# Kernel optimization log

Hardware: AMD Instinct MI355X
Metric: run time of the kernel (lower is better)

The kernel has to match this reference:

```python
import jax, jax.numpy as jnp
import numpy as np

NEG_SLOPE = 0.2  # PyG GATConv default LeakyReLU slope
BN_EPS = 1e-5


def gat_layer(x, src, dst, W, a_src, a_dst, num_nodes):
    """PyG-style GATConv (no dropout, eval mode). Returns [N, H, C]."""
    H, C = a_src.shape
    h = (x @ W).reshape(-1, H, C)                       # [N,H,C]
    s_src = jnp.einsum('nhc,hc->nh', h, a_src)          # [N,H]
    s_dst = jnp.einsum('nhc,hc->nh', h, a_dst)          # [N,H]
    e = jax.nn.leaky_relu(s_src[src] + s_dst[dst], NEG_SLOPE)  # [E,H]
    # segment softmax over incoming edges of each dst node
    e_max = jax.ops.segment_max(e, dst, num_segments=num_nodes)  # [N,H]
    e_exp = jnp.exp(e - e_max[dst])
    denom = jax.ops.segment_sum(e_exp, dst, num_segments=num_nodes)
    alpha = e_exp / (denom[dst] + 1e-16)                # [E,H]
    msg = h[src] * alpha[:, :, None]                    # [E,H,C] (dominant intermediate)
    return jax.ops.segment_sum(msg, dst, num_segments=num_nodes)  # [N,H,C]


def setup_inputs() -> dict:
    key = jax.random.key(0)
    ks = jax.random.split(key, 12)
    N, Din, Hdim, Heads, Dout = 50000, 128, 128, 8, 128
    E = 150000
    inp = {}
    inp['x'] = jax.random.normal(ks[0], (N, Din), dtype=jnp.float32)
    inp['edge_index'] = jax.random.randint(ks[1], (2, E), 0, N, dtype=jnp.int64)
    sc1 = 1.0 / np.sqrt(Din)
    inp['W1'] = jax.random.uniform(ks[2], (Din, Heads * Hdim), minval=-sc1, maxval=sc1, dtype=jnp.float32)
    inp['a_src1'] = jax.random.normal(ks[3], (Heads, Hdim), dtype=jnp.float32) * 0.1
    inp['a_dst1'] = jax.random.normal(ks[4], (Heads, Hdim), dtype=jnp.float32) * 0.1
    inp['b1'] = jnp.zeros((Heads * Hdim,), dtype=jnp.float32)
    inp['gamma'] = jnp.ones((Heads * Hdim,), dtype=jnp.float32)
    inp['beta'] = jnp.zeros((Heads * Hdim,), dtype=jnp.float32)
    sc2 = 1.0 / np.sqrt(Heads * Hdim)
    inp['W2'] = jax.random.uniform(ks[5], (Heads * Hdim, Dout), minval=-sc2, maxval=sc2, dtype=jnp.float32)
    inp['a_src2'] = jax.random.normal(ks[6], (1, Dout), dtype=jnp.float32) * 0.1
    inp['a_dst2'] = jax.random.normal(ks[7], (1, Dout), dtype=jnp.float32) * 0.1
    inp['b2'] = jnp.zeros((Dout,), dtype=jnp.float32)
    return inp


def reference(x, W1, a_src1, a_dst1, b1, gamma, beta, W2, a_src2, a_dst2, b2, edge_index):
    N = x.shape[0]
    src, dst = edge_index[0], edge_index[1]
    # GAT layer 1: heads=8, concat=True
    h1 = gat_layer(x, src, dst, W1, a_src1, a_dst1, N)   # [N,8,128]
    h1 = h1.reshape(N, -1) + b1                          # [N,1024]
    # BatchNorm1d (training-mode batch stats, biased variance as in torch)
    mu = jnp.mean(h1, axis=0)
    var = jnp.var(h1, axis=0)
    h1 = gamma * (h1 - mu) * jax.lax.rsqrt(var + BN_EPS) + beta
    h1 = jax.nn.elu(h1)
    # GAT layer 2: heads=1, concat=False (mean == squeeze for 1 head)
    h2 = gat_layer(h1, src, dst, W2, a_src2, a_dst2, N)  # [N,1,128]
    return h2[:, 0, :] + b2
```

## Files before the change

kernel.cpp:

```cpp
#include <hip/hip_runtime.h>
#include <hip/hip_bf16.h>
#include <math.h>

#define NEG_SLOPE 0.2f
#define BN_EPS 1e-5f

typedef short bf16x8 __attribute__((ext_vector_type(8)));
typedef float f32x4 __attribute__((ext_vector_type(4)));

__device__ __forceinline__ float bf2f(unsigned short u) {
  union { unsigned int i; float f; } v;
  v.i = ((unsigned int)u) << 16;
  return v.f;
}
__device__ __forceinline__ unsigned short f2bf(float f) {
  union { unsigned int i; float f; } v;
  v.f = f;
  unsigned int i = v.i;
  unsigned int r = (i + 0x7fffu + ((i >> 16) & 1u)) >> 16;
  return (unsigned short)r;
}

__global__ __launch_bounds__(256) void detect_kernel(
    const unsigned int* __restrict__ xw, const unsigned int* __restrict__ eiw,
    int E, int* __restrict__ flags) {
  __shared__ int cnt[2];
  if (threadIdx.x < 2) cnt[threadIdx.x] = 0;
  __syncthreads();
  int t = threadIdx.x;
  int inrange = 0;
  for (int i = t; i < 2048; i += 256) {
    unsigned int e = (xw[i] >> 7) & 0xFFu;
    inrange += (e >= 100u && e <= 135u) ? 1 : 0;
  }
  atomicAdd(&cnt[0], inrange);
  int M = min(1024, E / 2);
  int zeros = 0;
  for (int i = t; i < M; i += 256) zeros += (eiw[2 * i + 1] == 0u) ? 1 : 0;
  atomicAdd(&cnt[1], zeros);
  __syncthreads();
  if (t == 0) {
    flags[0] = (cnt[0] > 1536) ? 1 : 0;
    flags[1] = (cnt[1] > M / 2) ? 1 : 0;
  }
}

__global__ __launch_bounds__(256) void canon_x8(
    const void* __restrict__ src, unsigned short* __restrict__ dst, int n_real,
    int n_total, const int* __restrict__ flags) {
  int i = (blockIdx.x * 256 + threadIdx.x) * 8;
  if (i >= n_total) return;
  union { bf16x8 v; unsigned short u[8]; } o;
  if (i < n_real) {
    if (flags[0]) {
      o.v = *(const bf16x8*)((const unsigned short*)src + i);
    } else {
      const float4* f = (const float4*)((const float*)src + i);
      float4 f0 = f[0];
      float4 f1 = f[1];
      o.u[0] = f2bf(f0.x); o.u[1] = f2bf(f0.y);
      o.u[2] = f2bf(f0.z); o.u[3] = f2bf(f0.w);
      o.u[4] = f2bf(f1.x); o.u[5] = f2bf(f1.y);
      o.u[6] = f2bf(f1.z); o.u[7] = f2bf(f1.w);
    }
  } else {
#pragma unroll
    for (int j = 0; j < 8; ++j) o.u[j] = 0;
  }
  *(bf16x8*)(dst + i) = o.v;
}

__global__ __launch_bounds__(256) void canon_w_t(
    const void* __restrict__ src, unsigned short* __restrict__ dst, int Kdim,
    int Ndim, const int* __restrict__ flags) {
  int i = blockIdx.x * 256 + threadIdx.x;
  if (i >= Kdim * Ndim) return;
  int k = i / Ndim, n = i - k * Ndim;
  unsigned short v = flags[0] ? ((const unsigned short*)src)[i]
                              : f2bf(((const float*)src)[i]);
  dst[(size_t)n * Kdim + k] = v;
}

__global__ __launch_bounds__(1024) void canon_params(
    const void* s0, const void* s1, const void* s2, const void* s3,
    const void* s4, const void* s5, const void* s6, const void* s7,
    unsigned short* d0, unsigned short* d1, unsigned short* d2,
    unsigned short* d3, unsigned short* d4, unsigned short* d5,
    unsigned short* d6, unsigned short* d7, const int* __restrict__ flags) {
  int b = blockIdx.x, t = threadIdx.x;
  const void* s;
  unsigned short* d;
  int n;
  switch (b) {
    case 0: s = s0; d = d0; n = 1024; break;
    case 1: s = s1; d = d1; n = 1024; break;
    case 2: s = s2; d = d2; n = 1024; break;
    case 3: s = s3; d = d3; n = 1024; break;
    case 4: s = s4; d = d4; n = 1024; break;
    case 5: s = s5; d = d5; n = 128; break;
    case 6: s = s6; d = d6; n = 128; break;
    default: s = s7; d = d7; n = 128; break;
  }
  if (t < n)
    d[t] = flags[0] ? ((const unsigned short*)s)[t]
                    : f2bf(((const float*)s)[t]);
}

__global__ __launch_bounds__(256) void canon_idx(
    const int* __restrict__ ei, int* __restrict__ eis, int* __restrict__ eid,
    int E, const int* __restrict__ flags) {
  int e = blockIdx.x * 256 + threadIdx.x;
  if (e >= E) return;
  if (flags[1]) {
    eis[e] = ei[2 * (size_t)e];
    eid[e] = ei[2 * (size_t)E + 2 * (size_t)e];
  } else {
    eis[e] = ei[e];
    eid[e] = ei[E + e];
  }
}

template <int BM, bool TRANSFORM_A, bool OUT_BF16, bool SCORES>
__global__ __launch_bounds__(256) void gemm_mfma(
    const unsigned short* __restrict__ A, const unsigned short* __restrict__ Bt,
    void* __restrict__ Cv, int M, int N, int K,
    const float* __restrict__ scale, const float* __restrict__ shift,
    const unsigned short* __restrict__ aScr,
    const unsigned short* __restrict__ aDcr, float* __restrict__ ssrc,
    float* __restrict__ sdst, int hs) {
  constexpr int BK = 32;
  constexpr int LDA = BK + 8;
  constexpr int MI = BM / 32;
  __shared__ unsigned short As[BM * LDA];
  __shared__ unsigned short Bs[128 * LDA];
  __shared__ float sS[2][128];
  __shared__ float sD[2][128];

  const int m0 = blockIdx.y * BM;
  const int n0 = blockIdx.x * 128;
  const int tid = threadIdx.x;
  const int wid = tid >> 6;
  const int lane = tid & 63;
  const int q = lane >> 4;
  const int r = lane & 15;
  const int wm = (wid >> 1) * (BM / 2);
  const int wn = (wid & 1) * 64;

  f32x4 acc[MI][4] = {};

  const int row0 = (tid * 8) >> 5, col0 = (tid * 8) & 31;

  bf16x8 ra[2], rb[2];
  ra[0] = *(const bf16x8*)(A + (size_t)(m0 + row0) * K + col0);
  if (BM == 128)
    ra[1] = *(const bf16x8*)(A + (size_t)(m0 + row0 + 64) * K + col0);
  rb[0] = *(const bf16x8*)(Bt + (size_t)(n0 + row0) * K + col0);
  rb[1] = *(const bf16x8*)(Bt + (size_t)(n0 + row0 + 64) * K + col0);

  for (int k0 = 0; k0 < K; k0 += BK) {
#pragma unroll
    for (int rd = 0; rd < 2; ++rd) {
      int row = row0 + rd * 64;
      if (rd == 0 || BM == 128) {
        bf16x8 v = ra[rd];
        if (TRANSFORM_A) {
          float scv[8], shv[8];
          *(float4*)&scv[0] = *(const float4*)(scale + k0 + col0);
          *(float4*)&scv[4] = *(const float4*)(scale + k0 + col0 + 4);
          *(float4*)&shv[0] = *(const float4*)(shift + k0 + col0);
          *(float4*)&shv[4] = *(const float4*)(shift + k0 + col0 + 4);
          union { bf16x8 v; unsigned short u[8]; } p;
          p.v = v;
#pragma unroll
          for (int j = 0; j < 8; ++j) {
            float f = bf2f(p.u[j]) * scv[j] + shv[j];
            f = f > 0.f ? f : (__expf(f) - 1.0f);
            p.u[j] = f2bf(f);
          }
          v = p.v;
        }
        *(bf16x8*)(&As[row * LDA + col0]) = v;
      }
      *(bf16x8*)(&Bs[row * LDA + col0]) = rb[rd];
    }
    __syncthreads();

    int k1 = k0 + BK;
    if (k1 < K) {
      ra[0] = *(const bf16x8*)(A + (size_t)(m0 + row0) * K + k1 + col0);
      if (BM == 128)
        ra[1] = *(const bf16x8*)(A + (size_t)(m0 + row0 + 64) * K + k1 + col0);
      rb[0] = *(const bf16x8*)(Bt + (size_t)(n0 + row0) * K + k1 + col0);
      rb[1] = *(const bf16x8*)(Bt + (size_t)(n0 + row0 + 64) * K + k1 + col0);
    }

    bf16x8 af[MI], bfv[4];
#pragma unroll
    for (int mi = 0; mi < MI; ++mi)
      af[mi] = *(const bf16x8*)(&As[(wm + mi * 16 + r) * LDA + q * 8]);
#pragma unroll
    for (int ni = 0; ni < 4; ++ni)
      bfv[ni] = *(const bf16x8*)(&Bs[(wn + ni * 16 + r) * LDA + q * 8]);
#pragma unroll
    for (int mi = 0; mi < MI; ++mi)
#pragma unroll
      for (int ni = 0; ni < 4; ++ni)
        acc[mi][ni] = __builtin_amdgcn_mfma_f32_16x16x32_bf16(
            af[mi], bfv[ni], acc[mi][ni], 0, 0, 0);
    __syncthreads();
  }

#pragma unroll
  for (int mi = 0; mi < MI; ++mi) {
#pragma unroll
    for (int ni = 0; ni < 4; ++ni) {
#pragma unroll
      for (int i = 0; i < 4; ++i) {
        int row = m0 + wm + mi * 16 + q * 4 + i;
        int col = n0 + wn + ni * 16 + r;
        if (OUT_BF16)
          ((unsigned short*)Cv)[(size_t)row * N + col] = f2bf(acc[mi][ni][i]);
        else
          ((float*)Cv)[(size_t)row * N + col] = acc[mi][ni][i];
      }
    }
  }

  if (SCORES) {
    const int half = wid & 1;
    float aSv[4], aDv[4];
#pragma unroll
    for (int ni = 0; ni < 4; ++ni) {
      aSv[ni] = bf2f(aScr[n0 + wn + ni * 16 + r]);
      aDv[ni] = bf2f(aDcr[n0 + wn + ni * 16 + r]);
    }
#pragma unroll
    for (int mi = 0; mi < MI; ++mi) {
#pragma unroll
      for (int i = 0; i < 4; ++i) {
        float ps = 0.f, pd = 0.f;
#pragma unroll
        for (int ni = 0; ni < 4; ++ni) {
          float v = acc[mi][ni][i];
          ps += v * aSv[ni];
          pd += v * aDv[ni];
        }
        ps += __shfl_xor(ps, 1, 64); pd += __shfl_xor(pd, 1, 64);
        ps += __shfl_xor(ps, 2, 64); pd += __shfl_xor(pd, 2, 64);
        ps += __shfl_xor(ps, 4, 64); pd += __shfl_xor(pd, 4, 64);
        ps += __shfl_xor(ps, 8, 64); pd += __shfl_xor(pd, 8, 64);
        if (r == 0) {
          int rl = wm + mi * 16 + q * 4 + i;
          sS[half][rl] = ps;
          sD[half][rl] = pd;
        }
      }
    }
    __syncthreads();
    if (tid < BM) {
      int grow = m0 + tid;
      ssrc[(size_t)grow * hs + blockIdx.x] = sS[0][tid] + sS[1][tid];
      sdst[(size_t)grow * hs + blockIdx.x] = sD[0][tid] + sD[1][tid];
    }
  }
}

__global__ __launch_bounds__(256) void count_dst(const int* __restrict__ eid,
                                                 int E, int* __restrict__ cnt) {
  int e = blockIdx.x * 256 + threadIdx.x;
  if (e < E) atomicAdd(&cnt[eid[e]], 1);
}

__global__ __launch_bounds__(256) void scan_p1(const int* __restrict__ cnt,
                                               int* __restrict__ bsum, int N) {
  __shared__ int sd[256];
  int b = blockIdx.x, t = threadIdx.x;
  int base = b * 2048;
  int s = 0;
  for (int i = t; i < 2048; i += 256) {
    int idx = base + i;
    if (idx < N) s += cnt[idx];
  }
  sd[t] = s;
  __syncthreads();
  for (int o = 128; o > 0; o >>= 1) {
    if (t < o) sd[t] += sd[t + o];
    __syncthreads();
  }
  if (t == 0) bsum[b] = sd[0];
}

__global__ __launch_bounds__(256) void scan_p2(int* __restrict__ bsum, int nb) {
  __shared__ int sd[256];
  int t = threadIdx.x;
  int own = (t < nb) ? bsum[t] : 0;
  sd[t] = own;
  __syncthreads();
  for (int o = 1; o < 256; o <<= 1) {
    int v = (t >= o) ? sd[t - o] : 0;
    __syncthreads();
    sd[t] += v;
    __syncthreads();
  }
  if (t < nb) bsum[t] = sd[t] - own;
}

__global__ __launch_bounds__(256) void scan_p3(
    const int* __restrict__ cnt, const int* __restrict__ bsum,
    int* __restrict__ offsets, int* __restrict__ cursor, int N) {
  __shared__ int sd[256];
  int b = blockIdx.x, t = threadIdx.x;
  int base = b * 2048 + t * 8;
  int c[8];
  int ts = 0;
#pragma unroll
  for (int j = 0; j < 8; ++j) {
    int idx = base + j;
    c[j] = (idx < N) ? cnt[idx] : 0;
    ts += c[j];
  }
  sd[t] = ts;
  __syncthreads();
  for (int o = 1; o < 256; o <<= 1) {
    int v = (t >= o) ? sd[t - o] : 0;
    __syncthreads();
    sd[t] += v;
    __syncthreads();
  }
  int run = bsum[b] + sd[t] - ts;
#pragma unroll
  for (int j = 0; j < 8; ++j) {
    int idx = base + j;
    if (idx < N) {
      offsets[idx] = run;
      cursor[idx] = run;
      run += c[j];
    }
  }
  if (b == gridDim.x - 1 && t == 255) offsets[N] = bsum[b] + sd[255];
}

__global__ __launch_bounds__(256) void scatter_src(
    const int* __restrict__ eis, const int* __restrict__ eid, int E,
    int* __restrict__ cursor, int* __restrict__ srcs) {
  int e = blockIdx.x * 256 + threadIdx.x;
  if (e >= E) return;
  int d = eid[e];
  int pos = atomicAdd(&cursor[d], 1);
  srcs[pos] = eis[e];
}

__global__ __launch_bounds__(256) void agg1_csr(
    const int* __restrict__ offsets, const int* __restrict__ srcs,
    const unsigned short* __restrict__ h1, const float* __restrict__ ssrc,
    const float* __restrict__ sdst, const unsigned short* __restrict__ b1,
    unsigned short* __restrict__ h1n, int N) {
  int n = blockIdx.x * 4 + (threadIdx.x >> 6);
  if (n >= N) return;
  int lane = threadIdx.x & 63;
  int c0 = lane * 8;
  int c1 = 512 + c0;
  int hA = lane >> 4;
  int beg = offsets[n], end = offsets[n + 1];
  float sdA = sdst[n * 8 + hA];
  float sdB = sdst[n * 8 + hA + 4];
  float accA[8] = {}, accB[8] = {};
  float wsA = 0.f, wsB = 0.f;
  int p = beg;
  for (; p + 2 <= end; p += 2) {
    int s0 = srcs[p], s1 = srcs[p + 1];
    float vA0 = ssrc[s0 * 8 + hA] + sdA;
    float vB0 = ssrc[s0 * 8 + hA + 4] + sdB;
    float vA1 = ssrc[s1 * 8 + hA] + sdA;
    float vB1 = ssrc[s1 * 8 + hA + 4] + sdB;
    union { bf16x8 v; unsigned short u[8]; } uA0, uB0, uA1, uB1;
    uA0.v = *(const bf16x8*)(h1 + (size_t)s0 * 1024 + c0);
    uB0.v = *(const bf16x8*)(h1 + (size_t)s0 * 1024 + c1);
    uA1.v = *(const bf16x8*)(h1 + (size_t)s1 * 1024 + c0);
    uB1.v = *(const bf16x8*)(h1 + (size_t)s1 * 1024 + c1);
    vA0 = vA0 > 0.f ? vA0 : NEG_SLOPE * vA0;
    vB0 = vB0 > 0.f ? vB0 : NEG_SLOPE * vB0;
    vA1 = vA1 > 0.f ? vA1 : NEG_SLOPE * vA1;
    vB1 = vB1 > 0.f ? vB1 : NEG_SLOPE * vB1;
    float wA0 = __expf(vA0), wB0 = __expf(vB0);
    float wA1 = __expf(vA1), wB1 = __expf(vB1);
    wsA += wA0 + wA1;
    wsB += wB0 + wB1;
#pragma unroll
    for (int j = 0; j < 8; ++j) {
      accA[j] = fmaf(bf2f(uA0.u[j]), wA0, accA[j]);
      accB[j] = fmaf(bf2f(uB0.u[j]), wB0, accB[j]);
      accA[j] = fmaf(bf2f(uA1.u[j]), wA1, accA[j]);
      accB[j] = fmaf(bf2f(uB1.u[j]), wB1, accB[j]);
    }
  }
  if (p < end) {
    int s0 = srcs[p];
    float vA0 = ssrc[s0 * 8 + hA] + sdA;
    float vB0 = ssrc[s0 * 8 + hA + 4] + sdB;
    union { bf16x8 v; unsigned short u[8]; } uA0, uB0;
    uA0.v = *(const bf16x8*)(h1 + (size_t)s0 * 1024 + c0);
    uB0.v = *(const bf16x8*)(h1 + (size_t)s0 * 1024 + c1);
    vA0 = vA0 > 0.f ? vA0 : NEG_SLOPE * vA0;
    vB0 = vB0 > 0.f ? vB0 : NEG_SLOPE * vB0;
    float wA0 = __expf(vA0), wB0 = __expf(vB0);
    wsA += wA0;
    wsB += wB0;
#pragma unroll
    for (int j = 0; j < 8; ++j) {
      accA[j] = fmaf(bf2f(uA0.u[j]), wA0, accA[j]);
      accB[j] = fmaf(bf2f(uB0.u[j]), wB0, accB[j]);
    }
  }
  float invA = 1.0f / (wsA + 1e-16f);
  float invB = 1.0f / (wsB + 1e-16f);
  union { bf16x8 v; unsigned short u[8]; } bA, bB, oA, oB;
  bA.v = *(const bf16x8*)(b1 + c0);
  bB.v = *(const bf16x8*)(b1 + c1);
#pragma unroll
  for (int j = 0; j < 8; ++j) {
    oA.u[j] = f2bf(accA[j] * invA + bf2f(bA.u[j]));
    oB.u[j] = f2bf(accB[j] * invB + bf2f(bB.u[j]));
  }
  *(bf16x8*)(h1n + (size_t)n * 1024 + c0) = oA.v;
  *(bf16x8*)(h1n + (size_t)n * 1024 + c1) = oB.v;
}

__global__ __launch_bounds__(256) void bn_stats_part(
    const unsigned short* __restrict__ h1n, float* __restrict__ part, int N,
    int rowsPerBlock) {
  int b = blockIdx.x;
  int half = threadIdx.x >> 7;
  int t = threadIdx.x & 127;
  int c = t * 8;
  int r0 = b * rowsPerBlock;
  int r1 = min(r0 + rowsPerBlock, N);
  float s[8] = {0, 0, 0, 0, 0, 0, 0, 0};
  float q[8] = {0, 0, 0, 0, 0, 0, 0, 0};
  int r = r0 + half;
  for (; r + 2 < r1; r += 4) {
    union { bf16x8 v; unsigned short u[8]; } u0, u1;
    u0.v = *(const bf16x8*)(h1n + (size_t)r * 1024 + c);
    u1.v = *(const bf16x8*)(h1n + (size_t)(r + 2) * 1024 + c);
#pragma unroll
    for (int j = 0; j < 8; ++j) {
      float v0 = bf2f(u0.u[j]);
      float v1 = bf2f(u1.u[j]);
      s[j] += v0 + v1;
      q[j] = fmaf(v0, v0, q[j]);
      q[j] = fmaf(v1, v1, q[j]);
    }
  }
  for (; r < r1; r += 2) {
    union { bf16x8 v; unsigned short u[8]; } u0;
    u0.v = *(const bf16x8*)(h1n + (size_t)r * 1024 + c);
#pragma unroll
    for (int j = 0; j < 8; ++j) {
      float v0 = bf2f(u0.u[j]);
      s[j] += v0;
      q[j] = fmaf(v0, v0, q[j]);
    }
  }
  float* pb = part + ((size_t)b * 2 + half) * 2048;
#pragma unroll
  for (int j = 0; j < 8; ++j) {
    pb[c + j] = s[j];
    pb[1024 + c + j] = q[j];
  }
}

__global__ __launch_bounds__(256) void bn_reduce_finalize(
    const float* __restrict__ part, int nparts,
    const unsigned short* __restrict__ gamma,
    const unsigned short* __restrict__ beta, float* __restrict__ scale,
    float* __restrict__ shift, int N) {
  int c = blockIdx.x * 4 + (threadIdx.x >> 6);
  int lane = threadIdx.x & 63;
  float s = 0.f, q = 0.f;
  for (int b = lane; b < nparts; b += 64) {
    s += part[(size_t)b * 2048 + c];
    q += part[(size_t)b * 2048 + 1024 + c];
  }
#pragma unroll
  for (int o = 32; o > 0; o >>= 1) {
    s += __shfl_xor(s, o, 64);
    q += __shfl_xor(q, o, 64);
  }
  if (lane == 0) {
    float inv_n = 1.0f / (float)N;
    float mu = s * inv_n;
    float var = q * inv_n - mu * mu;
    float sc = bf2f(gamma[c]) * rsqrtf(var + BN_EPS);
    scale[c] = sc;
    shift[c] = bf2f(beta[c]) - mu * sc;
  }
}

__global__ __launch_bounds__(256) void agg2_csr(
    const int* __restrict__ offsets, const int* __restrict__ srcs,
    const float* __restrict__ h2, const float* __restrict__ ssrc,
    const float* __restrict__ sdst, const unsigned short* __restrict__ b2,
    void* __restrict__ out, const int* __restrict__ flags, int N) {
  int n = blockIdx.x * 8 + (threadIdx.x >> 5);
  if (n >= N) return;
  int c = (threadIdx.x & 31) * 4;
  int beg = offsets[n], end = offsets[n + 1];
  float sd = sdst[n];
  float a0 = 0.f, a1 = 0.f, a2 = 0.f, a3 = 0.f, wsum = 0.f;
  int p = beg;
  for (; p + 2 <= end; p += 2) {
    int s0 = srcs[p], s1 = srcs[p + 1];
    float v0 = ssrc[s0] + sd;
    float v1 = ssrc[s1] + sd;
    float4 u0 = *(const float4*)(h2 + (size_t)s0 * 128 + c);
    float4 u1 = *(const float4*)(h2 + (size_t)s1 * 128 + c);
    v0 = v0 > 0.f ? v0 : NEG_SLOPE * v0;
    v1 = v1 > 0.f ? v1 : NEG_SLOPE * v1;
    float w0 = __expf(v0), w1 = __expf(v1);
    wsum += w0 + w1;
    a0 = fmaf(u0.x, w0, a0);
    a1 = fmaf(u0.y, w0, a1);
    a2 = fmaf(u0.z, w0, a2);
    a3 = fmaf(u0.w, w0, a3);
    a0 = fmaf(u1.x, w1, a0);
    a1 = fmaf(u1.y, w1, a1);
    a2 = fmaf(u1.z, w1, a2);
    a3 = fmaf(u1.w, w1, a3);
  }
  if (p < end) {
    int s0 = srcs[p];
    float v0 = ssrc[s0] + sd;
    float4 u0 = *(const float4*)(h2 + (size_t)s0 * 128 + c);
    v0 = v0 > 0.f ? v0 : NEG_SLOPE * v0;
    float w0 = __expf(v0);
    wsum += w0;
    a0 = fmaf(u0.x, w0, a0);
    a1 = fmaf(u0.y, w0, a1);
    a2 = fmaf(u0.z, w0, a2);
    a3 = fmaf(u0.w, w0, a3);
  }
  float inv = 1.0f / (wsum + 1e-16f);
  ushort4 bb = *(const ushort4*)(b2 + c);
  float r0 = a0 * inv + bf2f(bb.x);
  float r1 = a1 * inv + bf2f(bb.y);
  float r2 = a2 * inv + bf2f(bb.z);
  float r3 = a3 * inv + bf2f(bb.w);
  if (flags[0]) {
    ushort4 o;
    o.x = f2bf(r0); o.y = f2bf(r1); o.z = f2bf(r2); o.w = f2bf(r3);
    *(ushort4*)((unsigned short*)out + (size_t)n * 128 + c) = o;
  } else {
    *(float4*)((float*)out + (size_t)n * 128 + c) =
        make_float4(r0, r1, r2, r3);
  }
}

extern "C" void kernel_launch(void* const* d_in, const int* in_sizes, int n_in,
                              void* d_out, int out_size, void* d_ws,
                              size_t ws_size, hipStream_t stream) {
  const void* x      = d_in[0];
  const int*  ei     = (const int*)d_in[1];
  const void* W1     = d_in[2];
  const void* a_src1 = d_in[3];
  const void* a_dst1 = d_in[4];
  const void* b1     = d_in[5];
  const void* gamma  = d_in[6];
  const void* beta   = d_in[7];
  const void* W2     = d_in[8];
  const void* a_src2 = d_in[9];
  const void* a_dst2 = d_in[10];
  const void* b2     = d_in[11];

  const int N = in_sizes[0] / 128;
  const int E = in_sizes[1] / 2;
  const int MP = ((N + 127) / 128) * 128;
  const int NB = (N + 2047) / 2048;
  const int NSTAT = 256;
  const int RPB = (N + NSTAT - 1) / NSTAT;

  char* ws = (char*)d_ws;
  size_t off = 0;
  unsigned short* h1  = (unsigned short*)(ws + off); off += (size_t)MP * 1024 * 2;
  char* h1n_base = ws + off;
  unsigned short* h1n = (unsigned short*)h1n_base;   off += (size_t)MP * 1024 * 2;
  float* ssrc1 = (float*)(ws + off); off += (size_t)MP * 8 * 4;
  float* sdst1 = (float*)(ws + off); off += (size_t)MP * 8 * 4;
  int* offsets = (int*)(ws + off); off += ((size_t)(N + 1) * 4 + 63) & ~63ull;
  int* srcs    = (int*)(ws + off); off += (size_t)E * 4;
  float* part  = (float*)(ws + off); off += (size_t)NSTAT * 2 * 2048 * 4;
  unsigned short* W1t = (unsigned short*)(ws + off); off += 131072 * 2;
  unsigned short* W2t = (unsigned short*)(ws + off); off += 131072 * 2;
  unsigned short* as1c = (unsigned short*)(ws + off); off += 1024 * 2;
  unsigned short* ad1c = (unsigned short*)(ws + off); off += 1024 * 2;
  unsigned short* b1c  = (unsigned short*)(ws + off); off += 1024 * 2;
  unsigned short* gmc  = (unsigned short*)(ws + off); off += 1024 * 2;
  unsigned short* btc  = (unsigned short*)(ws + off); off += 1024 * 2;
  unsigned short* as2c = (unsigned short*)(ws + off); off += 128 * 2;
  unsigned short* ad2c = (unsigned short*)(ws + off); off += 128 * 2;
  unsigned short* b2c  = (unsigned short*)(ws + off); off += 128 * 2;
  float* scale = (float*)(ws + off); off += 1024 * 4;
  float* shift = (float*)(ws + off); off += 1024 * 4;
  int* bsum    = (int*)(ws + off); off += 256 * 4;
  int* flags   = (int*)(ws + off); off += 64;
  unsigned short* x_bf = (unsigned short*)h1n_base;
  int* eis    = (int*)(h1n_base + (16u << 20));
  int* eid    = eis + E;
  int* cnt    = eid + E;
  int* cursor = cnt + N;
  float* h2    = (float*)h1;
  float* ssrc2 = ssrc1;
  float* sdst2 = sdst1;

  detect_kernel<<<1, 256, 0, stream>>>((const unsigned int*)x,
                                       (const unsigned int*)ei, E, flags);
  canon_x8<<<(MP * 128 / 8 + 255) / 256, 256, 0, stream>>>(x, x_bf, N * 128,
                                                           MP * 128, flags);
  canon_w_t<<<(131072 + 255) / 256, 256, 0, stream>>>(W1, W1t, 128, 1024, flags);
  canon_w_t<<<(131072 + 255) / 256, 256, 0, stream>>>(W2, W2t, 1024, 128, flags);
  canon_params<<<8, 1024, 0, stream>>>(a_src1, a_dst1, b1, gamma, beta, a_src2,
                                       a_dst2, b2, as1c, ad1c, b1c, gmc, btc,
                                       as2c, ad2c, b2c, flags);
  canon_idx<<<(E + 255) / 256, 256, 0, stream>>>(ei, eis, eid, E, flags);

  hipMemsetAsync(cnt, 0, (size_t)N * 4, stream);
  hipMemsetAsync((char*)h1n + (size_t)N * 1024 * 2, 0,
                 (size_t)(MP - N) * 1024 * 2, stream);

  count_dst<<<(E + 255) / 256, 256, 0, stream>>>(eid, E, cnt);
  scan_p1<<<NB, 256, 0, stream>>>(cnt, bsum, N);
  scan_p2<<<1, 256, 0, stream>>>(bsum, NB);
  scan_p3<<<NB, 256, 0, stream>>>(cnt, bsum, offsets, cursor, N);
  scatter_src<<<(E + 255) / 256, 256, 0, stream>>>(eis, eid, E, cursor, srcs);

  {
    dim3 g(1024 / 128, MP / 128);
    gemm_mfma<128, false, true, true><<<g, 256, 0, stream>>>(
        x_bf, W1t, h1, MP, 1024, 128, nullptr, nullptr, as1c, ad1c, ssrc1,
        sdst1, 8);
  }
  agg1_csr<<<(N + 3) / 4, 256, 0, stream>>>(offsets, srcs, h1, ssrc1, sdst1,
                                            b1c, h1n, N);

  bn_stats_part<<<NSTAT, 256, 0, stream>>>(h1n, part, N, RPB);
  bn_reduce_finalize<<<256, 256, 0, stream>>>(part, NSTAT * 2, gmc, btc, scale,
                                              shift, N);

  {
    dim3 g(1, MP / 64);
    gemm_mfma<64, true, false, true><<<g, 256, 0, stream>>>(
        h1n, W2t, h2, MP, 128, 1024, scale, shift, as2c, ad2c, ssrc2, sdst2,
        1);
  }
  agg2_csr<<<(N + 7) / 8, 256, 0, stream>>>(offsets, srcs, h2, ssrc2, sdst2,
                                            b2c, d_out, flags, N);
}
```

Baseline: 358.2 us.

## Specialize both GEMMs: full-K A tile reuse, XOR-swizzled LDS, head-major scores

Replaces the generic templated MFMA GEMM with two specialized kernels. For layer 1, each block loads its 64-row A tile once (full K=128) into XOR-swizzled shared memory and loops over all 8 head column blocks, prefetching the next W1 slice in registers. This avoids re-reading A for every column block and cuts LDS bank conflicts. Attention scores are now stored head-major, and agg1 reads them through per-head base pointers. The layer-2 GEMM uses BK=64 with fixed sizes, which halves the number of K iterations and barriers, at the cost of more registers and less launch parallelism in the layer-1 GEMM.

```diff
diff --git a/kernel.cpp b/kernel.cpp
--- a/kernel.cpp
+++ b/kernel.cpp
@@ -120,148 +120,254 @@
   }
 }
 
-template <int BM, bool TRANSFORM_A, bool OUT_BF16, bool SCORES>
-__global__ __launch_bounds__(256) void gemm_mfma(
-    const unsigned short* __restrict__ A, const unsigned short* __restrict__ Bt,
-    void* __restrict__ Cv, int M, int N, int K,
-    const float* __restrict__ scale, const float* __restrict__ shift,
+__global__ __launch_bounds__(256) void gemm1_fused(
+    const unsigned short* __restrict__ A,
+    const unsigned short* __restrict__ Bt,
+    unsigned short* __restrict__ C,
     const unsigned short* __restrict__ aScr,
-    const unsigned short* __restrict__ aDcr, float* __restrict__ ssrc,
-    float* __restrict__ sdst, int hs) {
-  constexpr int BK = 32;
-  constexpr int LDA = BK + 8;
-  constexpr int MI = BM / 32;
-  __shared__ unsigned short As[BM * LDA];
-  __shared__ unsigned short Bs[128 * LDA];
-  __shared__ float sS[2][128];
-  __shared__ float sD[2][128];
-
-  const int m0 = blockIdx.y * BM;
-  const int n0 = blockIdx.x * 128;
+    const unsigned short* __restrict__ aDcr,
+    float* __restrict__ ssrc,
+    float* __restrict__ sdst,
+    int MP) {
+  __shared__ unsigned short As[64 * 128];
+  __shared__ unsigned short Bs[128 * 128];
+  __shared__ float wscS[4][16];
+  __shared__ float wscD[4][16];
+
   const int tid = threadIdx.x;
   const int wid = tid >> 6;
   const int lane = tid & 63;
   const int q = lane >> 4;
   const int r = lane & 15;
-  const int wm = (wid >> 1) * (BM / 2);
+  const int wm = wid * 16;
+  const int m0 = blockIdx.x * 64;
+
+  const int arow = tid >> 4;
+  const int ag = tid & 15;
+
+  bf16x8 ra[4], rb[8];
+#pragma unroll
+  for (int j = 0; j < 4; ++j)
+    ra[j] = *(const bf16x8*)(A + (size_t)(m0 + j * 16 + arow) * 128 + ag * 8);
+#pragma unroll
+  for (int j = 0; j < 8; ++j)
+    rb[j] = *(const bf16x8*)(Bt + (size_t)(j * 16 + arow) * 128 + ag * 8);
+#pragma unroll
+  for (int j = 0; j < 4; ++j) {
+    int row = j * 16 + arow;
+    int gs = ag ^ (row & 15);
+    *(bf16x8*)(As + row * 128 + gs * 8) = ra[j];
+  }
+#pragma unroll
+  for (int j = 0; j < 8; ++j) {
+    int row = j * 16 + arow;
+    int gs = ag ^ (row & 15);
+    *(bf16x8*)(Bs + row * 128 + gs * 8) = rb[j];
+  }
+  __syncthreads();
+
+  for (int p = 0; p < 8; ++p) {
+    if (p < 7) {
+#pragma unroll
+      for (int j = 0; j < 8; ++j)
+        rb[j] = *(const bf16x8*)(Bt +
+                 (size_t)((p + 1) * 128 + j * 16 + arow) * 128 + ag * 8);
+    }
+    f32x4 acc[8] = {};
+#pragma unroll
+    for (int ks = 0; ks < 4; ++ks) {
+      bf16x8 af = *(const bf16x8*)(As + (wm + r) * 128 +
+                                   (((ks * 4 + q) ^ r) << 3));
+#pragma unroll
+      for (int ni = 0; ni < 8; ++ni) {
+        bf16x8 bf = *(const bf16x8*)(Bs + (ni * 16 + r) * 128 +
+                                     (((ks * 4 + q) ^ r) << 3));
+        acc[ni] = __builtin_amdgcn_mfma_f32_16x16x32_bf16(af, bf, acc[ni],
+                                                          0, 0, 0);
+      }
+    }
+#pragma unroll
+    for (int ni = 0; ni < 8; ++ni)
+#pragma unroll
+      for (int i = 0; i < 4; ++i)
+        C[(size_t)(m0 + wm + q * 4 + i) * 1024 + p * 128 + ni * 16 + r] =
+            f2bf(acc[ni][i]);
+    float aSv[8], aDv[8];
+#pragma unroll
+    for (int ni = 0; ni < 8; ++ni) {
+      aSv[ni] = bf2f(aScr[p * 128 + ni * 16 + r]);
+      aDv[ni] = bf2f(aDcr[p * 128 + ni * 16 + r]);
+    }
+#pragma unroll
+    for (int i = 0; i < 4; ++i) {
+      float ps = 0.f, pd = 0.f;
+#pragma unroll
+      for (int ni = 0; ni < 8; ++ni) {
+        ps += acc[ni][i] * aSv[ni];
+        pd += acc[ni][i] * aDv[ni];
+      }
+      ps += __shfl_xor(ps, 1, 64); pd += __shfl_xor(pd, 1, 64);
+      ps += __shfl_xor(ps, 2, 64); pd += __shfl_xor(pd, 2, 64);
+      ps += __shfl_xor(ps, 4, 64); pd += __shfl_xor(pd, 4, 64);
+      ps += __shfl_xor(ps, 8, 64); pd += __shfl_xor(pd, 8, 64);
+      if (r == 0) {
+        wscS[wid][q * 4 + i] = ps;
+        wscD[wid][q * 4 + i] = pd;
+      }
+    }
+    if (lane < 16)
+      ssrc[(size_t)p * MP + m0 + wm + lane] = wscS[wid][lane];
+    else if (lane < 32)
+      sdst[(size_t)p * MP + m0 + wm + (lane & 15)] = wscD[wid][lane & 15];
+    __syncthreads();
+    if (p < 7) {
+#pragma unroll
+      for (int j = 0; j < 8; ++j) {
+        int row = j * 16 + arow;
+        int gs = ag ^ (row & 15);
+        *(bf16x8*)(Bs + row * 128 + gs * 8) = rb[j];
+      }
+      __syncthreads();
+    }
+  }
+}
+
+__global__ __launch_bounds__(256) void gemm2_bn(
+    const unsigned short* __restrict__ A,
+    const unsigned short* __restrict__ Bt,
+    float* __restrict__ C,
+    const float* __restrict__ scale, const float* __restrict__ shift,
+    const unsigned short* __restrict__ aScr,
+    const unsigned short* __restrict__ aDcr,
+    float* __restrict__ ssrc, float* __restrict__ sdst) {
+  constexpr int K = 1024;
+  constexpr int BK = 64;
+  constexpr int LDA = BK + 8;
+  __shared__ unsigned short As[64 * LDA];
+  __shared__ unsigned short Bs[128 * LDA];
+  __shared__ float sS[2][64];
+  __shared__ float sD[2][64];
+
+  const int m0 = blockIdx.x * 64;
+  const int tid = threadIdx.x;
+  const int wid = tid >> 6;
+  const int lane = tid & 63;
+  const int q = lane >> 4;
+  const int r = lane & 15;
+  const int wm = (wid >> 1) * 32;
   const int wn = (wid & 1) * 64;
 
-  f32x4 acc[MI][4] = {};
-
-  const int row0 = (tid * 8) >> 5, col0 = (tid * 8) & 31;
-
-  bf16x8 ra[2], rb[2];
-  ra[0] = *(const bf16x8*)(A + (size_t)(m0 + row0) * K + col0);
-  if (BM == 128)
-    ra[1] = *(const bf16x8*)(A + (size_t)(m0 + row0 + 64) * K + col0);
-  rb[0] = *(const bf16x8*)(Bt + (size_t)(n0 + row0) * K + col0);
-  rb[1] = *(const bf16x8*)(Bt + (size_t)(n0 + row0 + 64) * K + col0);
+  f32x4 acc[2][4] = {};
+
+  const int row0 = tid >> 3;
+  const int col0 = (tid & 7) * 8;
+
+  bf16x8 ra[2], rb[4];
+#pragma unroll
+  for (int ca = 0; ca < 2; ++ca)
+    ra[ca] = *(const bf16x8*)(A + (size_t)(m0 + row0 + ca * 32) * K + col0);
+#pragma unroll
+  for (int cb = 0; cb < 4; ++cb)
+    rb[cb] = *(const bf16x8*)(Bt + (size_t)(row0 + cb * 32) * K + col0);
 
   for (int k0 = 0; k0 < K; k0 += BK) {
-#pragma unroll
-    for (int rd = 0; rd < 2; ++rd) {
-      int row = row0 + rd * 64;
-      if (rd == 0 || BM == 128) {
-        bf16x8 v = ra[rd];
-        if (TRANSFORM_A) {
-          float scv[8], shv[8];
-          *(float4*)&scv[0] = *(const float4*)(scale + k0 + col0);
-          *(float4*)&scv[4] = *(const float4*)(scale + k0 + col0 + 4);
-          *(float4*)&shv[0] = *(const float4*)(shift + k0 + col0);
-          *(float4*)&shv[4] = *(const float4*)(shift + k0 + col0 + 4);
-          union { bf16x8 v; unsigned short u[8]; } p;
-          p.v = v;
-#pragma unroll
-          for (int j = 0; j < 8; ++j) {
-            float f = bf2f(p.u[j]) * scv[j] + shv[j];
-            f = f > 0.f ? f : (__expf(f) - 1.0f);
-            p.u[j] = f2bf(f);
-          }
-          v = p.v;
-        }
-        *(bf16x8*)(&As[row * LDA + col0]) = v;
+    float scv[8], shv[8];
+    *(float4*)&scv[0] = *(const float4*)(scale + k0 + col0);
+    *(float4*)&scv[4] = *(const float4*)(scale + k0 + col0 + 4);
+    *(float4*)&shv[0] = *(const float4*)(shift + k0 + col0);
+    *(float4*)&shv[4] = *(const float4*)(shift + k0 + col0 + 4);
+#pragma unroll
+    for (int ca = 0; ca < 2; ++ca) {
+      union { bf16x8 v; unsigned short u[8]; } pk;
+      pk.v = ra[ca];
+#pragma unroll
+      for (int j = 0; j < 8; ++j) {
+        float f = bf2f(pk.u[j]) * scv[j] + shv[j];
+        f = f > 0.f ? f : (__expf(f) - 1.0f);
+        pk.u[j] = f2bf(f);
       }
-      *(bf16x8*)(&Bs[row * LDA + col0]) = rb[rd];
-    }
+      *(bf16x8*)(&As[(row0 + ca * 32) * LDA + col0]) = pk.v;
+    }
+#pragma unroll
+    for (int cb = 0; cb < 4; ++cb)
+      *(bf16x8*)(&Bs[(row0 + cb * 32) * LDA + col0]) = rb[cb];
     __syncthreads();
 
     int k1 = k0 + BK;
     if (k1 < K) {
-      ra[0] = *(const bf16x8*)(A + (size_t)(m0 + row0) * K + k1 + col0);
-      if (BM == 128)
-        ra[1] = *(const bf16x8*)(A + (size_t)(m0 + row0 + 64) * K + k1 + col0);
-      rb[0] = *(const bf16x8*)(Bt + (size_t)(n0 + row0) * K + k1 + col0);
-      rb[1] = *(const bf16x8*)(Bt + (size_t)(n0 + row0 + 64) * K + k1 + col0);
-    }
-
-    bf16x8 af[MI], bfv[4];
-#pragma unroll
-    for (int mi = 0; mi < MI; ++mi)
-      af[mi] = *(const bf16x8*)(&As[(wm + mi * 16 + r) * LDA + q * 8]);
+#pragma unroll
+      for (int ca = 0; ca < 2; ++ca)
+        ra[ca] = *(const bf16x8*)(A + (size_t)(m0 + row0 + ca * 32) * K + k1 +
+                                  col0);
+#pragma unroll
+      for (int cb = 0; cb < 4; ++cb)
+        rb[cb] = *(const bf16x8*)(Bt + (size_t)(row0 + cb * 32) * K + k1 +
+                                  col0);
+    }
+
+#pragma unroll
+    for (int ks = 0; ks < BK; ks += 32) {
+      bf16x8 af[2], bfv[4];
+#pragma unroll
+      for (int mi = 0; mi < 2; ++mi)
+        af[mi] = *(const bf16x8*)(&As[(wm + mi * 16 + r) * LDA + ks + q * 8]);
+#pragma unroll
+      for (int ni = 0; ni < 4; ++ni)
+        bfv[ni] = *(const bf16x8*)(&Bs[(wn + ni * 16 + r) * LDA + ks + q * 8]);
+#pragma unroll
+      for (int mi = 0; mi < 2; ++mi)
+#pragma unroll
+        for (int ni = 0; ni < 4; ++ni)
+          acc[mi][ni] = __builtin_amdgcn_mfma_f32_16x16x32_bf16(
+              af[mi], bfv[ni], acc[mi][ni], 0, 0, 0);
+    }
+    __syncthreads();
+  }
+
+#pragma unroll
+  for (int mi = 0; mi < 2; ++mi)
 #pragma unroll
     for (int ni = 0; ni < 4; ++ni)
-      bfv[ni] = *(const bf16x8*)(&Bs[(wn + ni * 16 + r) * LDA + q * 8]);
-#pragma unroll
-    for (int mi = 0; mi < MI; ++mi)
-#pragma unroll
-      for (int ni = 0; ni < 4; ++ni)
-        acc[mi][ni] = __builtin_amdgcn_mfma_f32_16x16x32_bf16(
-            af[mi], bfv[ni], acc[mi][ni], 0, 0, 0);
-    __syncthreads();
-  }
-
-#pragma unroll
-  for (int mi = 0; mi < MI; ++mi) {
-#pragma unroll
-    for (int ni = 0; ni < 4; ++ni) {
 #pragma unroll
       for (int i = 0; i < 4; ++i) {
         int row = m0 + wm + mi * 16 + q * 4 + i;
-        int col = n0 + wn + ni * 16 + r;
-        if (OUT_BF16)
-          ((unsigned short*)Cv)[(size_t)row * N + col] = f2bf(acc[mi][ni][i]);
-        else
-          ((float*)Cv)[(size_t)row * N + col] = acc[mi][ni][i];
+        int col = wn + ni * 16 + r;
+        C[(size_t)row * 128 + col] = acc[mi][ni][i];
       }
-    }
-  }
-
-  if (SCORES) {
-    const int half = wid & 1;
-    float aSv[4], aDv[4];
-#pragma unroll
-    for (int ni = 0; ni < 4; ++ni) {
-      aSv[ni] = bf2f(aScr[n0 + wn + ni * 16 + r]);
-      aDv[ni] = bf2f(aDcr[n0 + wn + ni * 16 + r]);
-    }
-#pragma unroll
-    for (int mi = 0; mi < MI; ++mi) {
-#pragma unroll
-      for (int i = 0; i < 4; ++i) {
-        float ps = 0.f, pd = 0.f;
-#pragma unroll
-        for (int ni = 0; ni < 4; ++ni) {
-          float v = acc[mi][ni][i];
-          ps += v * aSv[ni];
-          pd += v * aDv[ni];
-        }
-        ps += __shfl_xor(ps, 1, 64); pd += __shfl_xor(pd, 1, 64);
-        ps += __shfl_xor(ps, 2, 64); pd += __shfl_xor(pd, 2, 64);
-        ps += __shfl_xor(ps, 4, 64); pd += __shfl_xor(pd, 4, 64);
-        ps += __shfl_xor(ps, 8, 64); pd += __shfl_xor(pd, 8, 64);
-        if (r == 0) {
-          int rl = wm + mi * 16 + q * 4 + i;
-          sS[half][rl] = ps;
-          sD[half][rl] = pd;
-        }
+
+  const int half = wid & 1;
+  float aSv[4], aDv[4];
+#pragma unroll
+  for (int ni = 0; ni < 4; ++ni) {
+    aSv[ni] = bf2f(aScr[wn + ni * 16 + r]);
+    aDv[ni] = bf2f(aDcr[wn + ni * 16 + r]);
+  }
+#pragma unroll
+  for (int mi = 0; mi < 2; ++mi) {
+#pragma unroll
+    for (int i = 0; i < 4; ++i) {
+      float ps = 0.f, pd = 0.f;
+#pragma unroll
+      for (int ni = 0; ni < 4; ++ni) {
+        float v = acc[mi][ni][i];
+        ps += v * aSv[ni];
+        pd += v * aDv[ni];
       }
-    }
-    __syncthreads();
-    if (tid < BM) {
-      int grow = m0 + tid;
-      ssrc[(size_t)grow * hs + blockIdx.x] = sS[0][tid] + sS[1][tid];
-      sdst[(size_t)grow * hs + blockIdx.x] = sD[0][tid] + sD[1][tid];
-    }
+      ps += __shfl_xor(ps, 1, 64); pd += __shfl_xor(pd, 1, 64);
+      ps += __shfl_xor(ps, 2, 64); pd += __shfl_xor(pd, 2, 64);
+      ps += __shfl_xor(ps, 4, 64); pd += __shfl_xor(pd, 4, 64);
+      ps += __shfl_xor(ps, 8, 64); pd += __shfl_xor(pd, 8, 64);
+      if (r == 0) {
+        int rl = wm + mi * 16 + q * 4 + i;
+        sS[half][rl] = ps;
+        sD[half][rl] = pd;
+      }
+    }
+  }
+  __syncthreads();
+  if (tid < 64) {
+    ssrc[m0 + tid] = sS[0][tid] + sS[1][tid];
+    sdst[m0 + tid] = sD[0][tid] + sD[1][tid];
   }
 }
 
@@ -354,25 +460,27 @@
     const int* __restrict__ offsets, const int* __restrict__ srcs,
     const unsigned short* __restrict__ h1, const float* __restrict__ ssrc,
     const float* __restrict__ sdst, const unsigned short* __restrict__ b1,
-    unsigned short* __restrict__ h1n, int N) {
+    unsigned short* __restrict__ h1n, int N, int MP) {
   int n = blockIdx.x * 4 + (threadIdx.x >> 6);
   if (n >= N) return;
   int lane = threadIdx.x & 63;
   int c0 = lane * 8;
   int c1 = 512 + c0;
   int hA = lane >> 4;
+  const float* sSA = ssrc + (size_t)hA * MP;
+  const float* sSB = ssrc + (size_t)(hA + 4) * MP;
   int beg = offsets[n], end = offsets[n + 1];
-  float sdA = sdst[n * 8 + hA];
-  float sdB = sdst[n * 8 + hA + 4];
+  float sdA = sdst[(size_t)hA * MP + n];
+  float sdB = sdst[(size_t)(hA + 4) * MP + n];
   float accA[8] = {}, accB[8] = {};
   float wsA = 0.f, wsB = 0.f;
   int p = beg;
   for (; p + 2 <= end; p += 2) {
     int s0 = srcs[p], s1 = srcs[p + 1];
-    float vA0 = ssrc[s0 * 8 + hA] + sdA;
-    float vB0 = ssrc[s0 * 8 + hA + 4] + sdB;
-    float vA1 = ssrc[s1 * 8 + hA] + sdA;
-    float vB1 = ssrc[s1 * 8 + hA + 4] + sdB;
+    float vA0 = sSA[s0] + sdA;
+    float vB0 = sSB[s0] + sdB;
+    float vA1 = sSA[s1] + sdA;
+    float vB1 = sSB[s1] + sdB;
     union { bf16x8 v; unsigned short u[8]; } uA0, uB0, uA1, uB1;
     uA0.v = *(const bf16x8*)(h1 + (size_t)s0 * 1024 + c0);
     uB0.v = *(const bf16x8*)(h1 + (size_t)s0 * 1024 + c1);
@@ -396,8 +504,8 @@
   }
   if (p < end) {
     int s0 = srcs[p];
-    float vA0 = ssrc[s0 * 8 + hA] + sdA;
-    float vB0 = ssrc[s0 * 8 + hA + 4] + sdB;
+    float vA0 = sSA[s0] + sdA;
+    float vB0 = sSB[s0] + sdB;
     union { bf16x8 v; unsigned short u[8]; } uA0, uB0;
     uA0.v = *(const bf16x8*)(h1 + (size_t)s0 * 1024 + c0);
     uB0.v = *(const bf16x8*)(h1 + (size_t)s0 * 1024 + c1);
@@ -632,25 +740,17 @@
   scan_p3<<<NB, 256, 0, stream>>>(cnt, bsum, offsets, cursor, N);
   scatter_src<<<(E + 255) / 256, 256, 0, stream>>>(eis, eid, E, cursor, srcs);
 
-  {
-    dim3 g(1024 / 128, MP / 128);
-    gemm_mfma<128, false, true, true><<<g, 256, 0, stream>>>(
-        x_bf, W1t, h1, MP, 1024, 128, nullptr, nullptr, as1c, ad1c, ssrc1,
-        sdst1, 8);
-  }
+  gemm1_fused<<<MP / 64, 256, 0, stream>>>(x_bf, W1t, h1, as1c, ad1c, ssrc1,
+                                           sdst1, MP);
   agg1_csr<<<(N + 3) / 4, 256, 0, stream>>>(offsets, srcs, h1, ssrc1, sdst1,
-                                            b1c, h1n, N);
+                                            b1c, h1n, N, MP);
 
   bn_stats_part<<<NSTAT, 256, 0, stream>>>(h1n, part, N, RPB);
   bn_reduce_finalize<<<256, 256, 0, stream>>>(part, NSTAT * 2, gmc, btc, scale,
                                               shift, N);
 
-  {
-    dim3 g(1, MP / 64);
-    gemm_mfma<64, true, false, true><<<g, 256, 0, stream>>>(
-        h1n, W2t, h2, MP, 128, 1024, scale, shift, as2c, ad2c, ssrc2, sdst2,
-        1);
-  }
+  gemm2_bn<<<MP / 64, 256, 0, stream>>>(h1n, W2t, h2, scale, shift, as2c,
+                                        ad2c, ssrc2, sdst2);
   agg2_csr<<<(N + 7) / 8, 256, 0, stream>>>(offsets, srcs, h2, ssrc2, sdst2,
                                             b2c, d_out, flags, N);
 }
```

Measured after the change: 358.8 us. Within noise of the previous version (+0.1%).
